# Kernel optimization log

Hardware: AMD Instinct MI355X
Metric: run time of the kernel (lower is better)

Reference implementation:

```python
import jax, jax.numpy as jnp
import numpy as np

B, T, H, V = 32, 128, 1024, 32000


def setup_inputs() -> dict:
    key = jax.random.key(0)
    ks = jax.random.split(key, 10)
    s = 0.02
    return {
        "y_input": jax.random.normal(ks[0], (B, T), dtype=jnp.float32),
        "encoder_hidden_states": jax.random.normal(ks[1], (B, H), dtype=jnp.float32),
        "W_h": jax.random.normal(ks[2], (H, H), dtype=jnp.float32) * s,   # h_projection (no bias)
        "W_c": jax.random.normal(ks[3], (H, H), dtype=jnp.float32) * s,   # c_projection (no bias)
        "W_ih": jax.random.normal(ks[4], (4 * H, 1 + H), dtype=jnp.float32) * s,
        "W_hh": jax.random.normal(ks[5], (4 * H, H), dtype=jnp.float32) * s,
        "b_ih": jax.random.normal(ks[6], (4 * H,), dtype=jnp.float32) * s,
        "b_hh": jax.random.normal(ks[7], (4 * H,), dtype=jnp.float32) * s,
        "W_out": jax.random.normal(ks[8], (V, H), dtype=jnp.float32) * s,
        "b_out": jax.random.normal(ks[9], (V,), dtype=jnp.float32) * s,
    }


def reference(y_input, encoder_hidden_states, W_h, W_c, W_ih, W_hh, b_ih, b_hh, W_out, b_out):
    # init hidden/cell from encoder states (bias-free projections)
    h0 = encoder_hidden_states @ W_h.T  # [B, H]
    c0 = encoder_hidden_states @ W_c.T  # [B, H]

    def step(carry, x_t):
        h, c = carry
        ybar = jnp.concatenate([x_t[:, None], h], axis=-1)           # [B, 1+H]
        gates = ybar @ W_ih.T + b_ih + h @ W_hh.T + b_hh             # [B, 4H]
        i, f, g, o = jnp.split(gates, 4, axis=-1)                    # torch LSTMCell gate order
        i = jax.nn.sigmoid(i)
        f = jax.nn.sigmoid(f)
        g = jnp.tanh(g)
        o = jax.nn.sigmoid(o)
        c_new = f * c + i * g
        h_new = o * jnp.tanh(c_new)
        return (h_new, c_new), h_new

    _, hs = jax.lax.scan(step, (h0, c0), y_input.T)  # hs: [T, B, H]
    logits = hs @ W_out.T + b_out                    # [T, B, V]
    return jnp.transpose(logits, (1, 2, 0))          # [B, V, T]
```

## Files before the change

kernel.cpp:

```cpp
#include <hip/hip_runtime.h>
#include <hip/hip_bf16.h>
#include <stdint.h>

#define B_ 32
#define T_ 128
#define H_ 1024
#define V_ 32000
#define NBLK_REC 64

typedef unsigned short u16;
typedef __attribute__((ext_vector_type(8))) short short8;
typedef __attribute__((ext_vector_type(4))) float f32x4;

static __device__ __forceinline__ u16 f2bf(float f) {
    uint32_t u = __float_as_uint(f);
    uint32_t r = (u + 0x7FFFu + ((u >> 16) & 1u)) >> 16;
    return (u16)r;
}

static __device__ __forceinline__ float sigmf(float x) {
    return 1.0f / (1.0f + __expf(-x));
}

static __device__ __forceinline__ float tanh_f(float x) {
    x = fminf(fmaxf(x, -20.f), 20.f);
    float e = __expf(2.f * x);
    return (e - 1.f) / (e + 1.f);
}

static __device__ __forceinline__ void gload16(const void* g, void* l) {
    __builtin_amdgcn_global_load_lds(
        (const __attribute__((address_space(1))) uint32_t*)g,
        (__attribute__((address_space(3))) uint32_t*)(uint32_t)(uintptr_t)l,
        16, 0, 0);
}

__global__ void prep_w(const float* __restrict__ Wih, const float* __restrict__ Whh,
                       const float* __restrict__ bih, const float* __restrict__ bhh,
                       u16* __restrict__ Wc, float* __restrict__ wx, float* __restrict__ biasc,
                       unsigned* __restrict__ flags) {
    int idx = blockIdx.x * 256 + threadIdx.x;
    int r = idx >> 10, k = idx & 1023;
    float v = Wih[r * (H_ + 1) + 1 + k] + Whh[idx];
    Wc[idx] = f2bf(v);
    if (k == 0) {
        wx[r] = Wih[r * (H_ + 1)];
        biasc[r] = bih[r] + bhh[r];
    }
    if (idx < 2048) flags[idx] = 0u;
}

__global__ void prep_wout(const float* __restrict__ Wout, u16* __restrict__ Wo) {
    long long i = (long long)(blockIdx.x) * 256 + threadIdx.x;
    f32x4 v = *(const f32x4*)(Wout + i * 4);
    uint2 o;
    o.x = (uint32_t)f2bf(v[0]) | ((uint32_t)f2bf(v[1]) << 16);
    o.y = (uint32_t)f2bf(v[2]) | ((uint32_t)f2bf(v[3]) << 16);
    *(uint2*)(Wo + i * 4) = o;
}

__global__ void init_hc(const float* __restrict__ enc, const float* __restrict__ Wh,
                        const float* __restrict__ Wcp, u16* __restrict__ h0,
                        float* __restrict__ c0) {
    int gwid = blockIdx.x * 4 + (threadIdx.x >> 6);
    int lane = threadIdx.x & 63;
    int sel = gwid >> 10;
    int j = gwid & 1023;
    const float* W = sel ? Wcp : Wh;
    const float* wrow = W + (size_t)j * H_;
    f32x4 wv[4];
#pragma unroll
    for (int it = 0; it < 4; ++it)
        wv[it] = *(const f32x4*)(wrow + it * 256 + lane * 4);
#pragma unroll 2
    for (int b = 0; b < B_; ++b) {
        const float* erow = enc + (size_t)b * H_;
        float acc = 0.f;
#pragma unroll
        for (int it = 0; it < 4; ++it) {
            f32x4 ev = *(const f32x4*)(erow + it * 256 + lane * 4);
            acc += wv[it][0] * ev[0] + wv[it][1] * ev[1] + wv[it][2] * ev[2] + wv[it][3] * ev[3];
        }
#pragma unroll
        for (int s = 32; s >= 1; s >>= 1) acc += __shfl_xor(acc, s, 64);
        if (lane == 0) {
            if (sel) c0[(size_t)b * H_ + j] = acc;
            else     h0[(size_t)b * H_ + j] = f2bf(acc);
        }
    }
}

__global__ __launch_bounds__(512, 2) void fused_all(
    const u16* __restrict__ Wc, const float* __restrict__ wx,
    const float* __restrict__ biasc, const u16* __restrict__ h0,
    const float* __restrict__ c0, const float* __restrict__ y,
    u16* __restrict__ A, unsigned* __restrict__ flags,
    const u16* __restrict__ Wo, const float* __restrict__ bout,
    float* __restrict__ out) {
    __shared__ __align__(16) u16 sb[65536];

    int tid = threadIdx.x;
    int lane = tid & 63;

    if (blockIdx.x < NBLK_REC) {
        float* red = (float*)sb;
        float* cs  = red + 8 * 2112;
        float* wxs = cs + 16 * 33;
        float* bcs = wxs + 64;
        float* ys  = bcs + 64;

        int kw = tid >> 6;
        int bid = blockIdx.x;
        int j0 = bid * 16;
        int jl = lane & 15;
        int kc = (lane >> 4) * 8;
        int jlx = tid & 15, pb = tid >> 4;

        short8 afr[4][4];
        {
            const u16* abase = Wc + (size_t)(j0 + jl) * H_ + kw * 128 + kc;
#pragma unroll
            for (int g = 0; g < 4; ++g)
#pragma unroll
                for (int ks = 0; ks < 4; ++ks)
                    afr[g][ks] = *(const short8*)(abase + (size_t)g * H_ * H_ + ks * 32);
        }
#pragma unroll
        for (int g = 0; g < 4; ++g)
#pragma unroll
            for (int ks = 0; ks < 4; ++ks)
                asm volatile("" : "+v"(afr[g][ks]));

        if (tid < 64) {
            int g = tid >> 4, qq = tid & 15;
            wxs[tid] = wx[(size_t)g * H_ + j0 + qq];
            bcs[tid] = biasc[(size_t)g * H_ + j0 + qq];
        }
#pragma unroll
        for (int i = tid; i < B_ * T_; i += 512)
            ys[(i >> 7) * 129 + (i & 127)] = y[i];
        cs[jlx * 33 + pb] = c0[(size_t)pb * H_ + j0 + jlx];
        __syncthreads();

        for (int t = 0; t < T_; ++t) {
            const u16* hp = (t == 0) ? h0 : (A + (size_t)(t - 1) * B_ * H_);

            if (t > 0) {
                const unsigned* fp = &flags[(kw * 8 + (lane & 7)) * 32];
                unsigned target = (unsigned)t;
                int guard = 0;
                for (;;) {
                    unsigned v = __hip_atomic_load(fp, __ATOMIC_RELAXED, __HIP_MEMORY_SCOPE_AGENT);
                    if (__all(v >= target)) break;
                    if (++guard > 20000000) break;
                }
                __atomic_signal_fence(__ATOMIC_ACQUIRE);
            }

            short8 bf0[4], bf1[4];
            {
                const u16* hb = hp + (size_t)jl * H_ + kw * 128 + kc;
#pragma unroll
                for (int ks = 0; ks < 4; ++ks) {
                    bf0[ks] = *(const short8*)(hb + ks * 32);
                    bf1[ks] = *(const short8*)(hb + (size_t)16 * H_ + ks * 32);
                }
            }
            f32x4 acc[4][2] = {};
#pragma unroll
            for (int ks = 0; ks < 4; ++ks) {
#pragma unroll
                for (int g = 0; g < 4; ++g) {
                    acc[g][0] = __builtin_amdgcn_mfma_f32_16x16x32_bf16(afr[g][ks], bf0[ks], acc[g][0], 0, 0, 0);
                    acc[g][1] = __builtin_amdgcn_mfma_f32_16x16x32_bf16(afr[g][ks], bf1[ks], acc[g][1], 0, 0, 0);
                }
            }
            int r0 = (lane >> 4) * 4;
#pragma unroll
            for (int g = 0; g < 4; ++g)
#pragma unroll
                for (int bt = 0; bt < 2; ++bt)
#pragma unroll
                    for (int r = 0; r < 4; ++r)
                        red[kw * 2112 + (g * 16 + r0 + r) * 33 + bt * 16 + jl] = acc[g][bt][r];
            __syncthreads();

            {
                float yv = ys[pb * 129 + t];
                float pg[4];
#pragma unroll
                for (int g = 0; g < 4; ++g) {
                    int row = (g * 16 + jlx) * 33 + pb;
                    float sum = red[row];
#pragma unroll
                    for (int ww = 1; ww < 8; ++ww) sum += red[ww * 2112 + row];
                    pg[g] = sum + wxs[g * 16 + jlx] * yv + bcs[g * 16 + jlx];
                }
                float iv = sigmf(pg[0]);
                float fv = sigmf(pg[1]);
                float gv = tanh_f(pg[2]);
                float ov = sigmf(pg[3]);
                float cv = fv * cs[jlx * 33 + pb] + iv * gv;
                cs[jlx * 33 + pb] = cv;
                float hv = ov * tanh_f(cv);

                unsigned h16 = (unsigned)f2bf(hv);
                unsigned oth = (unsigned)__shfl((int)h16, lane + 1, 64);
                if (!(jlx & 1)) {
                    uint32_t pk = h16 | (oth << 16);
                    __hip_atomic_store((uint32_t*)(A + ((size_t)t * B_ + pb) * H_ + j0 + jlx),
                                       pk, __ATOMIC_RELAXED, __HIP_MEMORY_SCOPE_AGENT);
                }
            }
            __syncthreads();
            if (tid == 0)
                __hip_atomic_store(&flags[bid * 32], (unsigned)(t + 1),
                                   __ATOMIC_RELAXED, __HIP_MEMORY_SCOPE_AGENT);
        }
        return;
    }

    int orig = blockIdx.x - NBLK_REC;
    int tb = orig / 500;
    int wp = orig - tb * 500;
    int xcd = wp & 7, rest = wp >> 3;
    int wg = (xcd < 4 ? xcd * 63 : 252 + (xcd - 4) * 62) + rest;
    int bb = wg / 125;
    int nb = wg - bb * 125;
    int n0g = nb << 8;

    int wid = tid >> 6;
    int wm = wid >> 2, wn = wid & 3;
    int jl = lane & 15, kq = lane >> 4;

    f32x4 acc[8][4] = {};

    auto stage = [&](int tile, int h) {
        u16* dst = sb + ((tile & 1) << 15) + (h << 13) + tid * 8;
#pragma unroll
        for (int ld = 0; ld < 2; ++ld) {
            int p = tid + (ld << 9);
            int row = p >> 3;
            int c16 = (p & 7) ^ (row & 7);
            const u16* src;
            if (h < 2)
                src = A + ((size_t)(tb * 32 + (row & 31)) * B_
                           + (size_t)(bb * 8 + h * 4 + (row >> 5))) * H_
                        + tile * 64 + c16 * 8;
            else
                src = Wo + (size_t)(n0g + ((h - 2) << 7) + row) * H_
                         + tile * 64 + c16 * 8;
            gload16(src, dst + (ld << 12));
        }
    };

    stage(0, 2); stage(0, 3);

    if (wid == 0) {
        unsigned target = (unsigned)((tb + 1) * 32);
        const unsigned* fp = &flags[lane * 32];
        int guard = 0;
        for (;;) {
            unsigned v = __hip_atomic_load(fp, __ATOMIC_RELAXED, __HIP_MEMORY_SCOPE_AGENT);
            if (__all(v >= target)) break;
            __builtin_amdgcn_s_sleep(32);
            if (++guard > 20000000) break;
        }
        __atomic_signal_fence(__ATOMIC_ACQUIRE);
    }
    __builtin_amdgcn_s_barrier();

    stage(0, 0); stage(0, 1); stage(1, 0); stage(1, 2);
    asm volatile("s_waitcnt vmcnt(4)" ::: "memory");
    __builtin_amdgcn_s_barrier();

    const int NT = 16;
    for (int tile = 0; tile < NT; ++tile) {
        const u16* buf = sb + ((tile & 1) << 15);
#pragma unroll
        for (int q = 0; q < 4; ++q) {
            const int mh = q >> 1, nh = q & 1;
            short8 af[4][2], bfr[2][2];
            const u16* bufA = buf + (mh << 13);
            const u16* bufB = buf + (1 << 14) + (nh << 13);
#pragma unroll
            for (int i = 0; i < 4; ++i) {
                int row = wm * 64 + (i << 4) + jl;
                int rx = (row & 7) << 3;
#pragma unroll
                for (int k2 = 0; k2 < 2; ++k2)
                    af[i][k2] = *(const short8*)(bufA + row * 64 + (((k2 << 5) + (kq << 3)) ^ rx));
            }
#pragma unroll
            for (int i = 0; i < 2; ++i) {
                int row = wn * 32 + (i << 4) + jl;
                int rx = (row & 7) << 3;
#pragma unroll
                for (int k2 = 0; k2 < 2; ++k2)
                    bfr[i][k2] = *(const short8*)(bufB + row * 64 + (((k2 << 5) + (kq << 3)) ^ rx));
            }
            if (q == 0) { if (tile + 1 < NT) stage(tile + 1, 1); }
            if (q == 1) { if (tile + 1 < NT) stage(tile + 1, 3); }
            if (q == 2) { if (tile + 2 < NT) stage(tile + 2, 0); }
            if (q == 3) { if (tile + 2 < NT) stage(tile + 2, 2); }

            asm volatile("" ::: "memory");
            __builtin_amdgcn_s_barrier();
            asm volatile("" ::: "memory");
            __builtin_amdgcn_s_setprio(1);
#pragma unroll
            for (int i = 0; i < 4; ++i)
#pragma unroll
                for (int jn = 0; jn < 2; ++jn)
#pragma unroll
                    for (int k2 = 0; k2 < 2; ++k2)
                        acc[mh * 4 + i][nh * 2 + jn] =
                            __builtin_amdgcn_mfma_f32_16x16x32_bf16(
                                af[i][k2], bfr[jn][k2], acc[mh * 4 + i][nh * 2 + jn], 0, 0, 0);
            __builtin_amdgcn_s_setprio(0);
            if (q == 3) {
                if (tile < 14) asm volatile("s_waitcnt vmcnt(4)" ::: "memory");
                else           asm volatile("s_waitcnt vmcnt(0)" ::: "memory");
            }
            asm volatile("" ::: "memory");
            __builtin_amdgcn_s_barrier();
        }
    }

    __syncthreads();
    float* wsl = (float*)sb + wid * 2048;
#pragma unroll
    for (int nt = 0; nt < 4; ++nt) {
        {
            int n = n0g + ((nt >> 1) << 7) + wn * 32 + ((nt & 1) << 4) + jl;
            float bias = bout[n];
#pragma unroll
            for (int mt = 0; mt < 8; ++mt) {
                int mh = mt >> 2, i = mt & 3;
                int b2 = mh * 2 + (i >> 1);
                int g = ((i & 1) << 2) + kq;
                f32x4 v = acc[mt][nt];
                v[0] += bias; v[1] += bias; v[2] += bias; v[3] += bias;
                *(f32x4*)(wsl + jl * 128 + b2 * 32 + ((g ^ (jl & 7)) << 2)) = v;
            }
        }
#pragma unroll
        for (int rr = 0; rr < 2; ++rr) {
            int flat = lane * 2 + rr;
            int jr = flat >> 3;
            int b2r = (flat >> 1) & 3;
            int h2 = flat & 1;
            int n2 = n0g + ((nt >> 1) << 7) + wn * 32 + ((nt & 1) << 4) + jr;
            int bo = bb * 8 + (b2r >> 1) * 4 + wm * 2 + (b2r & 1);
            int t0 = tb * 32 + h2 * 16;
            float* dst = out + ((size_t)bo * V_ + n2) * T_ + t0;
            const float* sp = wsl + jr * 128 + b2r * 32;
#pragma unroll
            for (int gg = 0; gg < 4; ++gg) {
                int g2 = h2 * 4 + gg;
                f32x4 v = *(const f32x4*)(sp + ((g2 ^ (jr & 7)) << 2));
                *(f32x4*)(dst + (gg << 2)) = v;
            }
        }
    }
}

extern "C" void kernel_launch(void* const* d_in, const int* in_sizes, int n_in,
                              void* d_out, int out_size, void* d_ws, size_t ws_size,
                              hipStream_t stream) {
    const float* y    = (const float*)d_in[0];
    const float* enc  = (const float*)d_in[1];
    const float* Wh   = (const float*)d_in[2];
    const float* Wcp  = (const float*)d_in[3];
    const float* Wih  = (const float*)d_in[4];
    const float* Whh  = (const float*)d_in[5];
    const float* bih  = (const float*)d_in[6];
    const float* bhh  = (const float*)d_in[7];
    const float* Wout = (const float*)d_in[8];
    const float* bout = (const float*)d_in[9];

    uint8_t* ws = (uint8_t*)d_ws;
    u16*  Wcomb = (u16*)ws;
    u16*  Wo    = (u16*)(ws + 8388608);
    float* wx    = (float*)(ws + 8388608 + 65536000);
    float* biasc = wx + 4096;
    u16*  h0    = (u16*)(biasc + 4096);
    float* c     = (float*)(h0 + 32 * 1024);
    u16*  A     = (u16*)(c + 32 * 1024);
    unsigned* flags = (unsigned*)(A + (size_t)4096 * 1024);

    prep_w<<<16384, 256, 0, stream>>>(Wih, Whh, bih, bhh, Wcomb, wx, biasc, flags);
    prep_wout<<<32000, 256, 0, stream>>>(Wout, Wo);
    init_hc<<<512, 256, 0, stream>>>(enc, Wh, Wcp, h0, c);

    fused_all<<<NBLK_REC + 2000, 512, 0, stream>>>(
        Wcomb, wx, biasc, h0, c, y, A, flags, Wo, bout, (float*)d_out);
}
```

Before: 740.6 us.

## Merge prep kernels, raise recurrent block priority, store output tiles directly

Result: no change. 732.0 us (-1.2%).

```diff
diff --git a/kernel.cpp b/kernel.cpp
--- a/kernel.cpp
+++ b/kernel.cpp
@@ -35,57 +35,65 @@
         16, 0, 0);
 }
 
-__global__ void prep_w(const float* __restrict__ Wih, const float* __restrict__ Whh,
-                       const float* __restrict__ bih, const float* __restrict__ bhh,
-                       u16* __restrict__ Wc, float* __restrict__ wx, float* __restrict__ biasc,
-                       unsigned* __restrict__ flags) {
-    int idx = blockIdx.x * 256 + threadIdx.x;
-    int r = idx >> 10, k = idx & 1023;
-    float v = Wih[r * (H_ + 1) + 1 + k] + Whh[idx];
-    Wc[idx] = f2bf(v);
-    if (k == 0) {
-        wx[r] = Wih[r * (H_ + 1)];
-        biasc[r] = bih[r] + bhh[r];
-    }
-    if (idx < 2048) flags[idx] = 0u;
-}
-
-__global__ void prep_wout(const float* __restrict__ Wout, u16* __restrict__ Wo) {
-    long long i = (long long)(blockIdx.x) * 256 + threadIdx.x;
-    f32x4 v = *(const f32x4*)(Wout + i * 4);
-    uint2 o;
-    o.x = (uint32_t)f2bf(v[0]) | ((uint32_t)f2bf(v[1]) << 16);
-    o.y = (uint32_t)f2bf(v[2]) | ((uint32_t)f2bf(v[3]) << 16);
-    *(uint2*)(Wo + i * 4) = o;
-}
-
-__global__ void init_hc(const float* __restrict__ enc, const float* __restrict__ Wh,
-                        const float* __restrict__ Wcp, u16* __restrict__ h0,
-                        float* __restrict__ c0) {
-    int gwid = blockIdx.x * 4 + (threadIdx.x >> 6);
-    int lane = threadIdx.x & 63;
-    int sel = gwid >> 10;
-    int j = gwid & 1023;
-    const float* W = sel ? Wcp : Wh;
-    const float* wrow = W + (size_t)j * H_;
-    f32x4 wv[4];
-#pragma unroll
-    for (int it = 0; it < 4; ++it)
-        wv[it] = *(const f32x4*)(wrow + it * 256 + lane * 4);
+__global__ void prep_fused(const float* __restrict__ Wih, const float* __restrict__ Whh,
+                           const float* __restrict__ bih, const float* __restrict__ bhh,
+                           const float* __restrict__ Wout,
+                           const float* __restrict__ enc, const float* __restrict__ Wh,
+                           const float* __restrict__ Wcp,
+                           u16* __restrict__ Wc, float* __restrict__ wx,
+                           float* __restrict__ biasc, unsigned* __restrict__ flags,
+                           u16* __restrict__ Wo, u16* __restrict__ h0,
+                           float* __restrict__ c0) {
+    int blk = blockIdx.x;
+    int tid = threadIdx.x;
+
+    if (blk < 16384) {
+        int idx = blk * 256 + tid;
+        int r = idx >> 10, k = idx & 1023;
+        float v = Wih[r * (H_ + 1) + 1 + k] + Whh[idx];
+        Wc[idx] = f2bf(v);
+        if (k == 0) {
+            wx[r] = Wih[r * (H_ + 1)];
+            biasc[r] = bih[r] + bhh[r];
+        }
+        if (idx < 2048) flags[idx] = 0u;
+        return;
+    }
+    if (blk < 48384) {
+        long long i = (long long)(blk - 16384) * 256 + tid;
+        f32x4 v = *(const f32x4*)(Wout + i * 4);
+        uint2 o;
+        o.x = (uint32_t)f2bf(v[0]) | ((uint32_t)f2bf(v[1]) << 16);
+        o.y = (uint32_t)f2bf(v[2]) | ((uint32_t)f2bf(v[3]) << 16);
+        *(uint2*)(Wo + i * 4) = o;
+        return;
+    }
+    {
+        int gwid = (blk - 48384) * 4 + (tid >> 6);
+        int lane = tid & 63;
+        int sel = gwid >> 10;
+        int j = gwid & 1023;
+        const float* W = sel ? Wcp : Wh;
+        const float* wrow = W + (size_t)j * H_;
+        f32x4 wv[4];
+#pragma unroll
+        for (int it = 0; it < 4; ++it)
+            wv[it] = *(const f32x4*)(wrow + it * 256 + lane * 4);
 #pragma unroll 2
-    for (int b = 0; b < B_; ++b) {
-        const float* erow = enc + (size_t)b * H_;
-        float acc = 0.f;
-#pragma unroll
-        for (int it = 0; it < 4; ++it) {
-            f32x4 ev = *(const f32x4*)(erow + it * 256 + lane * 4);
-            acc += wv[it][0] * ev[0] + wv[it][1] * ev[1] + wv[it][2] * ev[2] + wv[it][3] * ev[3];
-        }
-#pragma unroll
-        for (int s = 32; s >= 1; s >>= 1) acc += __shfl_xor(acc, s, 64);
-        if (lane == 0) {
-            if (sel) c0[(size_t)b * H_ + j] = acc;
-            else     h0[(size_t)b * H_ + j] = f2bf(acc);
+        for (int b = 0; b < B_; ++b) {
+            const float* erow = enc + (size_t)b * H_;
+            float acc = 0.f;
+#pragma unroll
+            for (int it = 0; it < 4; ++it) {
+                f32x4 ev = *(const f32x4*)(erow + it * 256 + lane * 4);
+                acc += wv[it][0] * ev[0] + wv[it][1] * ev[1] + wv[it][2] * ev[2] + wv[it][3] * ev[3];
+            }
+#pragma unroll
+            for (int s = 32; s >= 1; s >>= 1) acc += __shfl_xor(acc, s, 64);
+            if (lane == 0) {
+                if (sel) c0[(size_t)b * H_ + j] = acc;
+                else     h0[(size_t)b * H_ + j] = f2bf(acc);
+            }
         }
     }
 }
@@ -103,6 +111,7 @@
     int lane = tid & 63;
 
     if (blockIdx.x < NBLK_REC) {
+        __builtin_amdgcn_s_setprio(2);
         float* red = (float*)sb;
         float* cs  = red + 8 * 2112;
         float* wxs = cs + 16 * 33;
@@ -327,40 +336,18 @@
         }
     }
 
-    __syncthreads();
-    float* wsl = (float*)sb + wid * 2048;
 #pragma unroll
     for (int nt = 0; nt < 4; ++nt) {
-        {
-            int n = n0g + ((nt >> 1) << 7) + wn * 32 + ((nt & 1) << 4) + jl;
-            float bias = bout[n];
-#pragma unroll
-            for (int mt = 0; mt < 8; ++mt) {
-                int mh = mt >> 2, i = mt & 3;
-                int b2 = mh * 2 + (i >> 1);
-                int g = ((i & 1) << 2) + kq;
-                f32x4 v = acc[mt][nt];
-                v[0] += bias; v[1] += bias; v[2] += bias; v[3] += bias;
-                *(f32x4*)(wsl + jl * 128 + b2 * 32 + ((g ^ (jl & 7)) << 2)) = v;
-            }
-        }
-#pragma unroll
-        for (int rr = 0; rr < 2; ++rr) {
-            int flat = lane * 2 + rr;
-            int jr = flat >> 3;
-            int b2r = (flat >> 1) & 3;
-            int h2 = flat & 1;
-            int n2 = n0g + ((nt >> 1) << 7) + wn * 32 + ((nt & 1) << 4) + jr;
-            int bo = bb * 8 + (b2r >> 1) * 4 + wm * 2 + (b2r & 1);
-            int t0 = tb * 32 + h2 * 16;
-            float* dst = out + ((size_t)bo * V_ + n2) * T_ + t0;
-            const float* sp = wsl + jr * 128 + b2r * 32;
-#pragma unroll
-            for (int gg = 0; gg < 4; ++gg) {
-                int g2 = h2 * 4 + gg;
-                f32x4 v = *(const f32x4*)(sp + ((g2 ^ (jr & 7)) << 2));
-                *(f32x4*)(dst + (gg << 2)) = v;
-            }
+        int n = n0g + ((nt >> 1) << 7) + wn * 32 + ((nt & 1) << 4) + jl;
+        float bias = bout[n];
+#pragma unroll
+        for (int mt = 0; mt < 8; ++mt) {
+            int mh = mt >> 2, i = mt & 3;
+            int bo = bb * 8 + mh * 4 + wm * 2 + (i >> 1);
+            f32x4 v = acc[mt][nt];
+            v[0] += bias; v[1] += bias; v[2] += bias; v[3] += bias;
+            float* dst = out + ((size_t)bo * V_ + n) * T_ + tb * 32 + ((i & 1) << 4) + (kq << 2);
+            *(f32x4*)dst = v;
         }
     }
 }
@@ -389,9 +376,8 @@
     u16*  A     = (u16*)(c + 32 * 1024);
     unsigned* flags = (unsigned*)(A + (size_t)4096 * 1024);
 
-    prep_w<<<16384, 256, 0, stream>>>(Wih, Whh, bih, bhh, Wcomb, wx, biasc, flags);
-    prep_wout<<<32000, 256, 0, stream>>>(Wout, Wo);
-    init_hc<<<512, 256, 0, stream>>>(enc, Wh, Wcp, h0, c);
+    prep_fused<<<48896, 256, 0, stream>>>(Wih, Whh, bih, bhh, Wout, enc, Wh, Wcp,
+                                          Wcomb, wx, biasc, flags, Wo, h0, c);
 
     fused_all<<<NBLK_REC + 2000, 512, 0, stream>>>(
         Wcomb, wx, biasc, h0, c, y, A, flags, Wo, bout, (float*)d_out);
```
